# Kernel optimization log

Hardware: AMD Instinct MI355X
Metric: run time of the kernel (lower is better)

## Reference

```python
import jax, jax.numpy as jnp
import numpy as np

B, T, C = 2, 2048, 2048
H, Hk, D = 32, 4, 64
N_REP = H // Hk
THETA = 10000.0


def _rope_tables():
    inv_freq = 1.0 / (THETA ** (np.arange(0, D, 2, dtype=np.float64) / D))  # [D/2]
    t = np.arange(T, dtype=np.float64)
    freqs = np.outer(t, inv_freq)                # [T, D/2]
    emb = np.repeat(freqs, 2, axis=-1)           # interleaved [T, D]
    return jnp.asarray(np.cos(emb), jnp.float32), jnp.asarray(np.sin(emb), jnp.float32)


def setup_inputs() -> dict:
    key = jax.random.key(0)
    kx, kq, kk, kv, ko = jax.random.split(key, 5)
    scale = 0.02
    x = jax.random.normal(kx, (B, T, C), jnp.float32)
    wq = jax.random.normal(kq, (H * D, C), jnp.float32) * scale
    wk = jax.random.normal(kk, (Hk * D, C), jnp.float32) * scale
    wv = jax.random.normal(kv, (Hk * D, C), jnp.float32) * scale
    wo = jax.random.normal(ko, (C, H * D), jnp.float32) * scale
    cos, sin = _rope_tables()
    return {"x": x, "cos": cos, "sin": sin, "wq": wq, "wk": wk, "wv": wv, "wo": wo}


def _apply_rope(x, cos, sin):
    # x: [B, h, T, D]; cos/sin: [T, D] interleaved
    x1 = x[..., 0::2]
    x2 = x[..., 1::2]
    rot = jnp.stack([-x2, x1], axis=-1).reshape(x.shape)
    return x * cos[None, None] + rot * sin[None, None]


def reference(x, cos, sin, wq, wk, wv, wo):
    q = (x @ wq.T).reshape(B, T, H, D).transpose(0, 2, 1, 3)    # [B,H,T,D]
    k = (x @ wk.T).reshape(B, T, Hk, D).transpose(0, 2, 1, 3)   # [B,Hk,T,D]
    v = (x @ wv.T).reshape(B, T, Hk, D).transpose(0, 2, 1, 3)   # [B,Hk,T,D]
    q = _apply_rope(q, cos, sin)
    k = _apply_rope(k, cos, sin)
    # new_cache = (k, v) pre-repeat
    kr = jnp.repeat(k, N_REP, axis=1)                            # [B,H,T,D]
    vr = jnp.repeat(v, N_REP, axis=1)
    scores = jnp.einsum('bhtd,bhsd->bhts', q, kr) / jnp.sqrt(jnp.float32(D))
    mask = jnp.tril(jnp.ones((T, T), dtype=bool))                # causal (kv_cache is None)
    scores = jnp.where(mask, scores, jnp.finfo(scores.dtype).min)
    attn = jax.nn.softmax(scores, axis=-1)
    o = jnp.einsum('bhts,bhsd->bhtd', attn, vr)
    o = o.transpose(0, 2, 1, 3).reshape(B, T, H * D)
    return (o @ wo.T, k, v)
```

## Files before the change

kernel.cpp:

```cpp
#include <hip/hip_runtime.h>
#include <hip/hip_bf16.h>

#define B_ 2
#define T_ 2048
#define C_ 2048
#define H_ 32
#define HK_ 4
#define D_ 64

typedef __attribute__((ext_vector_type(4)))  float f32x4;
typedef __attribute__((ext_vector_type(2)))  float f32x2;
typedef __attribute__((ext_vector_type(16))) float f32x16;
typedef __attribute__((ext_vector_type(8)))  short bf16x8;

static __device__ __forceinline__ unsigned short f2bf(float f) {
  union { __hip_bfloat16 h; unsigned short s; } u;
  u.h = __float2bfloat16(f);
  return u.s;
}
static __device__ __forceinline__ float bf2f(unsigned short s) {
  union { unsigned int u; float f; } u; u.u = ((unsigned int)s) << 16; return u.f;
}
static __device__ __forceinline__ unsigned int cvtpk(float lo, float hi) {
  unsigned int r;
  asm("v_cvt_pk_bf16_f32 %0, %1, %2" : "=v"(r) : "v"(lo), "v"(hi));
  return r;
}

#define GLD16(gp, lp) __builtin_amdgcn_global_load_lds( \
    (const __attribute__((address_space(1))) unsigned int*)(gp), \
    (__attribute__((address_space(3))) unsigned int*)(unsigned int)(uintptr_t)(lp), 16, 0, 0)

__global__ void f32_to_bf16(const float* __restrict__ src, unsigned short* __restrict__ dst, int n4) {
  const int i = blockIdx.x * blockDim.x + threadIdx.x;
  if (i >= n4) return;
  f32x4 v = *(const f32x4*)(src + 4 * (size_t)i);
  ushort4 o;
  o.x = f2bf(v[0]); o.y = f2bf(v[1]); o.z = f2bf(v[2]); o.w = f2bf(v[3]);
  *(ushort4*)(dst + 4 * (size_t)i) = o;
}

template<bool BF16OUT>
__global__ __launch_bounds__(256, 3)
void gemm3(const unsigned short* __restrict__ A, const unsigned short* __restrict__ W,
           void* __restrict__ Cout, int M, int N, int K) {
  __shared__ unsigned short As[3][128 * 32];
  __shared__ unsigned short Ws[3][128 * 32];

  const int tid  = threadIdx.x;
  const int lane = tid & 63;
  const int w    = tid >> 6;
  const int wm   = w >> 1, wn = w & 1;
  const int g    = lane >> 4;
  const int lr   = lane & 15;

  const int bm = blockIdx.y * 128;
  const int bn = blockIdx.x * 128;

  const int srow = tid >> 2;
  const int sc   = (tid & 3) ^ (srow & 3);
  const unsigned short* Ag = A + (size_t)(bm + srow) * K + sc * 8;
  const unsigned short* Wg = W + (size_t)(bn + srow) * K + sc * 8;

#define STAGE3(buf, k0) do { \
    GLD16(Ag + (k0),                  &As[buf][       w * 512]); \
    GLD16(Ag + (size_t)64 * K + (k0), &As[buf][2048 + w * 512]); \
    GLD16(Wg + (k0),                  &Ws[buf][       w * 512]); \
    GLD16(Wg + (size_t)64 * K + (k0), &Ws[buf][2048 + w * 512]); \
  } while (0)

  f32x4 acc[4][4] = {};

  const int nt = K >> 5;
  STAGE3(0, 0);
  STAGE3(1, 32);

  for (int t = 0; t < nt; ++t) {
    if (t + 1 < nt) asm volatile("s_waitcnt vmcnt(4)" ::: "memory");
    else            asm volatile("s_waitcnt vmcnt(0)" ::: "memory");
    asm volatile("s_barrier" ::: "memory");

    if (t + 2 < nt) {
      const int nb = (t + 2) % 3;
      STAGE3(nb, (size_t)(t + 2) * 32);
    }

    const unsigned short* At = &As[t % 3][0];
    const unsigned short* Wt = &Ws[t % 3][0];

    bf16x8 af[4], wf[4];
#pragma unroll
    for (int m = 0; m < 4; m++) {
      const int row = wm * 64 + m * 16 + lr;
      af[m] = *(const bf16x8*)&At[row * 32 + ((g ^ (row & 3)) << 3)];
    }
#pragma unroll
    for (int n = 0; n < 4; n++) {
      const int row = wn * 64 + n * 16 + lr;
      wf[n] = *(const bf16x8*)&Wt[row * 32 + ((g ^ (row & 3)) << 3)];
    }
    __builtin_amdgcn_s_setprio(1);
#pragma unroll
    for (int m = 0; m < 4; m++)
#pragma unroll
      for (int n = 0; n < 4; n++)
        acc[m][n] = __builtin_amdgcn_mfma_f32_16x16x32_bf16(af[m], wf[n], acc[m][n], 0, 0, 0);
    __builtin_amdgcn_s_setprio(0);
  }
#undef STAGE3

#pragma unroll
  for (int m = 0; m < 4; m++) {
    const int row = bm + wm * 64 + m * 16 + g * 4;
#pragma unroll
    for (int n = 0; n < 4; n++) {
      const int col = bn + wn * 64 + n * 16 + lr;
#pragma unroll
      for (int r = 0; r < 4; r++) {
        if (BF16OUT)
          ((unsigned short*)Cout)[(size_t)(row + r) * N + col] = f2bf(acc[m][n][r]);
        else
          ((float*)Cout)[(size_t)(row + r) * N + col] = acc[m][n][r];
      }
    }
  }
}

__global__ void gqa_rope_q(const unsigned short* __restrict__ qkv,
                           const float* __restrict__ cosT,
                           const float* __restrict__ sinT,
                           unsigned short* __restrict__ qb) {
  const int idx = blockIdx.x * blockDim.x + threadIdx.x;
  const int i  = idx & 31;
  const int h  = (idx >> 5) & 31;
  const int bt = idx >> 10;
  const int t  = bt & (T_ - 1);
  const int b  = bt >> 11;

  const unsigned int qv = *(const unsigned int*)(qkv + (size_t)bt * 2560 + h * D_ + 2 * i);
  const float x1 = bf2f((unsigned short)(qv & 0xffff));
  const float x2 = bf2f((unsigned short)(qv >> 16));
  const float c = cosT[t * D_ + 2 * i];
  const float s = sinT[t * D_ + 2 * i];
  const float o0 = x1 * c - x2 * s;
  const float o1 = x2 * c + x1 * s;
  const size_t o = ((size_t)(b * H_ + h) * T_ + t) * D_ + 2 * i;
  *(unsigned int*)(qb + o) = (unsigned int)f2bf(o0) | ((unsigned int)f2bf(o1) << 16);
}

__global__ void gqa_rope_k(const unsigned short* __restrict__ qkv,
                           const float* __restrict__ cosT,
                           const float* __restrict__ sinT,
                           float* __restrict__ kout,
                           unsigned short* __restrict__ kb) {
  const int idx = blockIdx.x * blockDim.x + threadIdx.x;
  const int i  = idx & 31;
  const int hk = (idx >> 5) & 3;
  const int bt = idx >> 7;
  const int t  = bt & (T_ - 1);
  const int b  = bt >> 11;

  const unsigned int kv = *(const unsigned int*)(qkv + (size_t)bt * 2560 + 2048 + hk * D_ + 2 * i);
  const float x1 = bf2f((unsigned short)(kv & 0xffff));
  const float x2 = bf2f((unsigned short)(kv >> 16));
  const float c = cosT[t * D_ + 2 * i];
  const float s = sinT[t * D_ + 2 * i];
  const float o0 = x1 * c - x2 * s;
  const float o1 = x2 * c + x1 * s;
  const size_t o = ((size_t)(b * HK_ + hk) * T_ + t) * D_ + 2 * i;
  f32x2 ov; ov[0] = o0; ov[1] = o1;
  *(f32x2*)(kout + o) = ov;
  *(unsigned int*)(kb + o) = (unsigned int)f2bf(o0) | ((unsigned int)f2bf(o1) << 16);
}

__global__ void gqa_v_reorder(const unsigned short* __restrict__ qkv,
                              float* __restrict__ vout,
                              unsigned short* __restrict__ vt) {
  const int idx = blockIdx.x * blockDim.x + threadIdx.x;
  const int d  = idx & 63;
  const int hk = (idx >> 6) & 3;
  const int bt = idx >> 8;
  const int t  = bt & (T_ - 1);
  const int b  = bt >> 11;

  const unsigned short v = qkv[(size_t)bt * 2560 + 2304 + hk * D_ + d];
  vout[((size_t)(b * HK_ + hk) * T_ + t) * D_ + d] = bf2f(v);

  const int tm   = t & 15;
  const int tpos = (t & ~15) | ((tm & 3) + ((tm >> 3) << 2) + ((tm & 4) << 1));
  vt[((size_t)(b * HK_ + hk) * D_ + d) * T_ + tpos] = v;
}

__global__ __launch_bounds__(512, 4)
void gqa_attn4(const unsigned short* __restrict__ qb,
               const unsigned short* __restrict__ kb,
               const unsigned short* __restrict__ vt,
               unsigned short* __restrict__ ob) {
  __shared__ unsigned short Ks[3][4096];
  __shared__ unsigned short Vs[3][4096];

  const int tid  = threadIdx.x;
  const int lane = tid & 63;
  const int w    = tid >> 6;
  const int qi   = lane & 31;
  const int hi   = lane >> 5;

  const int qt = 63 - (int)(blockIdx.x >> 3);
  const int go = blockIdx.x & 7;
  const int b  = go >> 2;
  const int hk = go & 3;
  const int h  = hk * 8 + w;
  const int bh = b * H_ + h;

  const int qbase = qt * 32;
  const int qrow  = qbase + qi;

  const unsigned short* qptr = qb + ((size_t)bh * T_ + qrow) * D_ + 8 * hi;
  bf16x8 qf[4];
#pragma unroll
  for (int c = 0; c < 4; c++) qf[c] = *(const bf16x8*)(qptr + 16 * c);

  const int srow   = lane >> 3;
  const int schunk = (lane & 7) ^ srow;
  const int krow   = 8 * w + srow;
  const unsigned short* gK = kb + (size_t)(b * HK_ + hk) * T_ * D_ + (size_t)krow * D_ + schunk * 8;
  const unsigned short* gV = vt + (size_t)(b * HK_ + hk) * D_ * T_ + (size_t)krow * T_ + schunk * 8;
  unsigned short* ldsK = &Ks[0][w * 512];
  unsigned short* ldsV = &Vs[0][w * 512];

#define STAGE_KV(pp, kk0) do { \
    GLD16(gK + (size_t)(kk0) * D_, ldsK + (pp) * 4096); \
    GLD16(gV + (kk0),              ldsV + (pp) * 4096); \
  } while (0)

  f32x16 o0 = {}, o1 = {};
  float m = -1e30f, l = 0.f;
  float c1 = 0.f;
  const float SC   = 0.125f * 1.44269504089f;
  const float THRR = 44.3614195f;
  const int   swz  = qi & 7;

  const int nt = ((qbase + 31) >> 6) + 1;
  STAGE_KV(0, 0);
  if (nt > 1) STAGE_KV(1, 64);

  int p = 0;
  for (int it = 0; it < nt; ++it) {
    const int kb0 = it * 64;
    const bool last = (it == nt - 1);
    const bool has1 = (kb0 + 32 <= qbase + 31);

    asm volatile("s_waitcnt lgkmcnt(0)" ::: "memory");
    if (it + 1 < nt) asm volatile("s_waitcnt vmcnt(2)" ::: "memory");
    else             asm volatile("s_waitcnt vmcnt(0)" ::: "memory");
    asm volatile("s_barrier" ::: "memory");
    if (it + 2 < nt) STAGE_KV((p + 2 > 2) ? p - 1 : p + 2, kb0 + 128);

    const unsigned short* Kt = &Ks[0][0] + p * 4096;
    const unsigned short* Vt = &Vs[0][0] + p * 4096;

    f32x16 st0 = {}, st1 = {};
    __builtin_amdgcn_s_setprio(1);
#pragma unroll
    for (int c = 0; c < 4; c++) {
      bf16x8 kf = *(const bf16x8*)&Kt[qi * 64 + (((hi + 2 * c) ^ swz) << 3)];
      st0 = __builtin_amdgcn_mfma_f32_32x32x16_bf16(kf, qf[c], st0, 0, 0, 0);
    }
    if (!last || has1) {
#pragma unroll
      for (int c = 0; c < 4; c++) {
        bf16x8 kf = *(const bf16x8*)&Kt[(32 + qi) * 64 + (((hi + 2 * c) ^ swz) << 3)];
        st1 = __builtin_amdgcn_mfma_f32_32x32x16_bf16(kf, qf[c], st1, 0, 0, 0);
      }
    }
    __builtin_amdgcn_s_setprio(0);

    if (last) {
#pragma unroll
      for (int r = 0; r < 16; ++r) {
        const int key = kb0 + (r & 3) + 8 * (r >> 2) + 4 * hi;
        st0[r] = (key      <= qrow) ? st0[r] : -1e30f;
        st1[r] = (key + 32 <= qrow) ? st1[r] : -1e30f;
      }
    }

    float tmax = fmaxf(st0[0], st0[1]);
#pragma unroll
    for (int r = 2; r < 16; ++r) tmax = fmaxf(tmax, st0[r]);
#pragma unroll
    for (int r = 0; r < 16; ++r) tmax = fmaxf(tmax, st1[r]);
    tmax = fmaxf(tmax, __shfl_xor(tmax, 32));

    if (!__all(tmax <= m + THRR)) {
      const float mnew  = fmaxf(m, tmax);
      const float al    = __builtin_amdgcn_exp2f((m - mnew) * SC);
#pragma unroll
      for (int r = 0; r < 16; ++r) { o0[r] *= al; o1[r] *= al; }
      l *= al;
      m  = mnew;
      c1 = -m * SC;
    }

    float sum = 0.f;
#pragma unroll
    for (int r = 0; r < 16; ++r) { float pv = __builtin_amdgcn_exp2f(__builtin_fmaf(st0[r], SC, c1)); st0[r] = pv; sum += pv; }
#pragma unroll
    for (int r = 0; r < 16; ++r) { float pv = __builtin_amdgcn_exp2f(__builtin_fmaf(st1[r], SC, c1)); st1[r] = pv; sum += pv; }
    sum += __shfl_xor(sum, 32);
    l += sum;

    union U8 { bf16x8 v; unsigned int u[4]; };
    U8 pf[4];
#pragma unroll
    for (int j = 0; j < 4; ++j) {
      pf[0].u[j] = cvtpk(st0[2 * j],     st0[2 * j + 1]);
      pf[1].u[j] = cvtpk(st0[8 + 2 * j], st0[8 + 2 * j + 1]);
      pf[2].u[j] = cvtpk(st1[2 * j],     st1[2 * j + 1]);
      pf[3].u[j] = cvtpk(st1[8 + 2 * j], st1[8 + 2 * j + 1]);
    }

    const int ncf = (!last || has1) ? 4 : 2;
    __builtin_amdgcn_s_setprio(1);
#pragma unroll
    for (int dh = 0; dh < 2; ++dh) {
      const unsigned short* Vrow = &Vt[(dh * 32 + qi) * 64];
      f32x16 oc = dh ? o1 : o0;
#pragma unroll
      for (int c = 0; c < 4; ++c) {
        if (c >= ncf) break;
        bf16x8 vf = *(const bf16x8*)&Vrow[(((2 * c + hi) ^ swz) << 3)];
        oc = __builtin_amdgcn_mfma_f32_32x32x16_bf16(vf, pf[c].v, oc, 0, 0, 0);
      }
      if (dh) o1 = oc; else o0 = oc;
    }
    __builtin_amdgcn_s_setprio(0);

    p = (p > 1) ? 0 : p + 1;
  }

  const float inv = 1.0f / l;
  unsigned short* orow = ob + (size_t)(b * T_ + qrow) * (H_ * D_) + h * D_;
#pragma unroll
  for (int dh = 0; dh < 2; ++dh) {
    const f32x16 ov = dh ? o1 : o0;
#pragma unroll
    for (int rg = 0; rg < 4; ++rg) {
      const int d0 = 32 * dh + 8 * rg + 4 * hi;
      ushort4 pk;
      pk.x = f2bf(ov[4 * rg + 0] * inv);
      pk.y = f2bf(ov[4 * rg + 1] * inv);
      pk.z = f2bf(ov[4 * rg + 2] * inv);
      pk.w = f2bf(ov[4 * rg + 3] * inv);
      *(ushort4*)(orow + d0) = pk;
    }
  }
#undef STAGE_KV
}

extern "C" void kernel_launch(void* const* d_in, const int* in_sizes, int n_in,
                              void* d_out, int out_size, void* d_ws, size_t ws_size,
                              hipStream_t stream) {
  const float* x    = (const float*)d_in[0];
  const float* cosT = (const float*)d_in[1];
  const float* sinT = (const float*)d_in[2];
  const float* wq   = (const float*)d_in[3];
  const float* wk   = (const float*)d_in[4];
  const float* wv   = (const float*)d_in[5];
  const float* wo   = (const float*)d_in[6];

  float* y    = (float*)d_out;
  float* kout = (float*)d_out + (size_t)B_ * T_ * C_;
  float* vout = kout + (size_t)B_ * HK_ * T_ * D_;

  char* ws = (char*)d_ws;
  unsigned short* x_bf   = (unsigned short*)(ws);
  unsigned short* q_bf   = x_bf;
  unsigned short* wqkv   = (unsigned short*)(ws + 16777216);
  unsigned short* k_bf   = wqkv;
  unsigned short* v_t    = (unsigned short*)(ws + 18874368);
  unsigned short* qkv_bf = (unsigned short*)(ws + 27262976);
  unsigned short* o_bf   = qkv_bf;
  unsigned short* wo_bf  = (unsigned short*)(ws + 48234496);

  const int M = B_ * T_;

  f32_to_bf16<<<8192, 256, 0, stream>>>(x,  x_bf, 2097152);
  f32_to_bf16<<<4096, 256, 0, stream>>>(wq, wqkv,                 1048576);
  f32_to_bf16<<<512,  256, 0, stream>>>(wk, wqkv + 2048 * 2048,   131072);
  f32_to_bf16<<<512,  256, 0, stream>>>(wv, wqkv + 2304 * 2048,   131072);

  gemm3<true><<<dim3(2560 / 128, M / 128), 256, 0, stream>>>(x_bf, wqkv, qkv_bf, M, 2560, C_);

  gqa_rope_q<<<16384, 256, 0, stream>>>(qkv_bf, cosT, sinT, q_bf);
  gqa_rope_k<<<2048,  256, 0, stream>>>(qkv_bf, cosT, sinT, kout, k_bf);
  gqa_v_reorder<<<4096, 256, 0, stream>>>(qkv_bf, vout, v_t);

  f32_to_bf16<<<4096, 256, 0, stream>>>(wo, wo_bf, 1048576);

  gqa_attn4<<<512, 512, 0, stream>>>(q_bf, k_bf, v_t, o_bf);

  gemm3<false><<<dim3(C_ / 128, M / 128), 256, 0, stream>>>(o_bf, wo_bf, y, M, C_, H_ * D_);
}
```

Baseline: 209.2 us.

## Replace 128x128 triple-buffered GEMM with 128x256 double-buffered 512-thread GEMM

Both projection GEMMs now use a 128x256 block tile with 8 waves, a K-step of 64 instead of 32, and 8-way XOR swizzling in LDS. The pipeline drops from three buffers to two and waits for all loads (vmcnt(0)) before each barrier. The larger N tile raises reuse of the A tile and cuts the number of barriers per K. In exchange it uses more LDS per block and launches fewer blocks (320 and 256), which may leave parts of the 256-CU device underused and exposes load latency more.

```diff
diff --git a/kernel.cpp b/kernel.cpp
--- a/kernel.cpp
+++ b/kernel.cpp
@@ -41,73 +41,72 @@
 }
 
 template<bool BF16OUT>
-__global__ __launch_bounds__(256, 3)
-void gemm3(const unsigned short* __restrict__ A, const unsigned short* __restrict__ W,
-           void* __restrict__ Cout, int M, int N, int K) {
-  __shared__ unsigned short As[3][128 * 32];
-  __shared__ unsigned short Ws[3][128 * 32];
+__global__ __launch_bounds__(512, 2)
+void gemm256(const unsigned short* __restrict__ A, const unsigned short* __restrict__ W,
+             void* __restrict__ Cout, int M, int N, int K) {
+  __shared__ unsigned short As[2][128 * 64];
+  __shared__ unsigned short Bs[2][256 * 64];
 
   const int tid  = threadIdx.x;
   const int lane = tid & 63;
   const int w    = tid >> 6;
-  const int wm   = w >> 1, wn = w & 1;
+  const int wm   = w >> 2;
+  const int wn   = w & 3;
   const int g    = lane >> 4;
   const int lr   = lane & 15;
 
   const int bm = blockIdx.y * 128;
-  const int bn = blockIdx.x * 128;
-
-  const int srow = tid >> 2;
-  const int sc   = (tid & 3) ^ (srow & 3);
-  const unsigned short* Ag = A + (size_t)(bm + srow) * K + sc * 8;
-  const unsigned short* Wg = W + (size_t)(bn + srow) * K + sc * 8;
-
-#define STAGE3(buf, k0) do { \
-    GLD16(Ag + (k0),                  &As[buf][       w * 512]); \
-    GLD16(Ag + (size_t)64 * K + (k0), &As[buf][2048 + w * 512]); \
-    GLD16(Wg + (k0),                  &Ws[buf][       w * 512]); \
-    GLD16(Wg + (size_t)64 * K + (k0), &Ws[buf][2048 + w * 512]); \
+  const int bn = blockIdx.x * 256;
+
+  const int sr8 = lane >> 3;
+  const int sch = (lane & 7) ^ sr8;
+  const unsigned short* Ag = A + (size_t)(bm + w * 8 + sr8) * K + sch * 8;
+  const unsigned short* Wg = W + (size_t)(bn + w * 8 + sr8) * K + sch * 8;
+
+#define STG(buf, k0) do { \
+    GLD16(Ag + (k0),                   &As[buf][(      w * 8) * 64]); \
+    GLD16(Ag + (size_t)64  * K + (k0), &As[buf][(64  + w * 8) * 64]); \
+    GLD16(Wg + (k0),                   &Bs[buf][(      w * 8) * 64]); \
+    GLD16(Wg + (size_t)64  * K + (k0), &Bs[buf][(64  + w * 8) * 64]); \
+    GLD16(Wg + (size_t)128 * K + (k0), &Bs[buf][(128 + w * 8) * 64]); \
+    GLD16(Wg + (size_t)192 * K + (k0), &Bs[buf][(192 + w * 8) * 64]); \
   } while (0)
 
   f32x4 acc[4][4] = {};
-
-  const int nt = K >> 5;
-  STAGE3(0, 0);
-  STAGE3(1, 32);
+  const int nt = K >> 6;
+  STG(0, 0);
 
   for (int t = 0; t < nt; ++t) {
-    if (t + 1 < nt) asm volatile("s_waitcnt vmcnt(4)" ::: "memory");
-    else            asm volatile("s_waitcnt vmcnt(0)" ::: "memory");
-    asm volatile("s_barrier" ::: "memory");
-
-    if (t + 2 < nt) {
-      const int nb = (t + 2) % 3;
-      STAGE3(nb, (size_t)(t + 2) * 32);
-    }
-
-    const unsigned short* At = &As[t % 3][0];
-    const unsigned short* Wt = &Ws[t % 3][0];
-
-    bf16x8 af[4], wf[4];
-#pragma unroll
-    for (int m = 0; m < 4; m++) {
-      const int row = wm * 64 + m * 16 + lr;
-      af[m] = *(const bf16x8*)&At[row * 32 + ((g ^ (row & 3)) << 3)];
-    }
-#pragma unroll
-    for (int n = 0; n < 4; n++) {
-      const int row = wn * 64 + n * 16 + lr;
-      wf[n] = *(const bf16x8*)&Wt[row * 32 + ((g ^ (row & 3)) << 3)];
-    }
-    __builtin_amdgcn_s_setprio(1);
-#pragma unroll
-    for (int m = 0; m < 4; m++)
-#pragma unroll
-      for (int n = 0; n < 4; n++)
-        acc[m][n] = __builtin_amdgcn_mfma_f32_16x16x32_bf16(af[m], wf[n], acc[m][n], 0, 0, 0);
-    __builtin_amdgcn_s_setprio(0);
+    const int p = t & 1;
+    asm volatile("s_waitcnt vmcnt(0)" ::: "memory");
+    __builtin_amdgcn_s_barrier();
+    if (t + 1 < nt) STG(p ^ 1, (t + 1) << 6);
+
+    const unsigned short* At = &As[p][0];
+    const unsigned short* Bt = &Bs[p][0];
+#pragma unroll
+    for (int kh = 0; kh < 2; ++kh) {
+      bf16x8 af[4], wf[4];
+#pragma unroll
+      for (int m = 0; m < 4; m++) {
+        const int row = wm * 64 + m * 16 + lr;
+        af[m] = *(const bf16x8*)&At[row * 64 + (((g + 4 * kh) ^ (row & 7)) << 3)];
+      }
+#pragma unroll
+      for (int n = 0; n < 4; n++) {
+        const int row = wn * 64 + n * 16 + lr;
+        wf[n] = *(const bf16x8*)&Bt[row * 64 + (((g + 4 * kh) ^ (row & 7)) << 3)];
+      }
+      __builtin_amdgcn_s_setprio(1);
+#pragma unroll
+      for (int m = 0; m < 4; m++)
+#pragma unroll
+        for (int n = 0; n < 4; n++)
+          acc[m][n] = __builtin_amdgcn_mfma_f32_16x16x32_bf16(af[m], wf[n], acc[m][n], 0, 0, 0);
+      __builtin_amdgcn_s_setprio(0);
+    }
   }
-#undef STAGE3
+#undef STG
 
 #pragma unroll
   for (int m = 0; m < 4; m++) {
@@ -389,7 +388,7 @@
   f32_to_bf16<<<512,  256, 0, stream>>>(wk, wqkv + 2048 * 2048,   131072);
   f32_to_bf16<<<512,  256, 0, stream>>>(wv, wqkv + 2304 * 2048,   131072);
 
-  gemm3<true><<<dim3(2560 / 128, M / 128), 256, 0, stream>>>(x_bf, wqkv, qkv_bf, M, 2560, C_);
+  gemm256<true><<<dim3(2560 / 256, M / 128), 512, 0, stream>>>(x_bf, wqkv, qkv_bf, M, 2560, C_);
 
   gqa_rope_q<<<16384, 256, 0, stream>>>(qkv_bf, cosT, sinT, q_bf);
   gqa_rope_k<<<2048,  256, 0, stream>>>(qkv_bf, cosT, sinT, kout, k_bf);
@@ -399,5 +398,5 @@
 
   gqa_attn4<<<512, 512, 0, stream>>>(q_bf, k_bf, v_t, o_bf);
 
-  gemm3<false><<<dim3(C_ / 128, M / 128), 256, 0, stream>>>(o_bf, wo_bf, y, M, C_, H_ * D_);
-}
+  gemm256<false><<<dim3(C_ / 256, M / 128), 512, 0, stream>>>(o_bf, wo_bf, y, M, C_, H_ * D_);
+}
```

Result: no change. 206.8 us (-1.1%).

## Pair causal query tiles per attention block and merge weight conversion kernels

Applied to the files above, without the earlier changes.

The attention kernel now gives each block two query tiles, one from the far end and one from the near end of the causal range. Both tiles run over the same staged K/V tiles, so causal work is even across blocks and each K/V load is used twice. The grid shrinks to 256 blocks with launch bounds lowered to 2, which costs per-wave register pressure and occupancy. Separately, the five fp32-to-bf16 conversion launches become one combined kernel to cut launch overhead.

```diff
diff --git a/kernel.cpp b/kernel.cpp
--- a/kernel.cpp
+++ b/kernel.cpp
@@ -31,13 +31,25 @@
     (const __attribute__((address_space(1))) unsigned int*)(gp), \
     (__attribute__((address_space(3))) unsigned int*)(unsigned int)(uintptr_t)(lp), 16, 0, 0)
 
-__global__ void f32_to_bf16(const float* __restrict__ src, unsigned short* __restrict__ dst, int n4) {
+__global__ void conv_all(const float* __restrict__ x,  const float* __restrict__ wq,
+                         const float* __restrict__ wk, const float* __restrict__ wv,
+                         const float* __restrict__ wo,
+                         unsigned short* __restrict__ x_bf,
+                         unsigned short* __restrict__ wqkv,
+                         unsigned short* __restrict__ wo_bf) {
   const int i = blockIdx.x * blockDim.x + threadIdx.x;
-  if (i >= n4) return;
-  f32x4 v = *(const f32x4*)(src + 4 * (size_t)i);
+  const float* src;
+  unsigned short* dst;
+  int off;
+  if (i < 2097152)      { src = x;  dst = x_bf;                  off = i; }
+  else if (i < 3145728) { src = wq; dst = wqkv;                  off = i - 2097152; }
+  else if (i < 3276800) { src = wk; dst = wqkv + 2048 * 2048;    off = i - 3145728; }
+  else if (i < 3407872) { src = wv; dst = wqkv + 2304 * 2048;    off = i - 3276800; }
+  else                  { src = wo; dst = wo_bf;                 off = i - 3407872; }
+  f32x4 v = *(const f32x4*)(src + 4 * (size_t)off);
   ushort4 o;
   o.x = f2bf(v[0]); o.y = f2bf(v[1]); o.z = f2bf(v[2]); o.w = f2bf(v[3]);
-  *(ushort4*)(dst + 4 * (size_t)i) = o;
+  *(ushort4*)(dst + 4 * (size_t)off) = o;
 }
 
 template<bool BF16OUT>
@@ -191,8 +203,96 @@
   vt[((size_t)(b * HK_ + hk) * D_ + d) * T_ + tpos] = v;
 }
 
-__global__ __launch_bounds__(512, 4)
-void gqa_attn4(const unsigned short* __restrict__ qb,
+static __device__ __forceinline__ void attn_qstep(
+    const unsigned short* __restrict__ Kt, const unsigned short* __restrict__ Vt,
+    const bf16x8 (&qf)[4], f32x16& o0, f32x16& o1,
+    float& m, float& l, float& c1,
+    const int qrow, const int kb0, const bool last,
+    const int qi, const int hi, const int swz) {
+  const float SC   = 0.125f * 1.44269504089f;
+  const float THRR = 44.3614195f;
+  const int  qtop  = (qrow & ~31) + 31;
+  const bool has1  = (kb0 + 32 <= qtop);
+
+  f32x16 st0 = {}, st1 = {};
+  __builtin_amdgcn_s_setprio(1);
+#pragma unroll
+  for (int c = 0; c < 4; c++) {
+    bf16x8 kf = *(const bf16x8*)&Kt[qi * 64 + (((hi + 2 * c) ^ swz) << 3)];
+    st0 = __builtin_amdgcn_mfma_f32_32x32x16_bf16(kf, qf[c], st0, 0, 0, 0);
+  }
+  if (!last || has1) {
+#pragma unroll
+    for (int c = 0; c < 4; c++) {
+      bf16x8 kf = *(const bf16x8*)&Kt[(32 + qi) * 64 + (((hi + 2 * c) ^ swz) << 3)];
+      st1 = __builtin_amdgcn_mfma_f32_32x32x16_bf16(kf, qf[c], st1, 0, 0, 0);
+    }
+  }
+  __builtin_amdgcn_s_setprio(0);
+
+  if (last) {
+#pragma unroll
+    for (int r = 0; r < 16; ++r) {
+      const int key = kb0 + (r & 3) + 8 * (r >> 2) + 4 * hi;
+      st0[r] = (key      <= qrow) ? st0[r] : -1e30f;
+      st1[r] = (key + 32 <= qrow) ? st1[r] : -1e30f;
+    }
+  }
+
+  float tmax = fmaxf(st0[0], st0[1]);
+#pragma unroll
+  for (int r = 2; r < 16; ++r) tmax = fmaxf(tmax, st0[r]);
+#pragma unroll
+  for (int r = 0; r < 16; ++r) tmax = fmaxf(tmax, st1[r]);
+  tmax = fmaxf(tmax, __shfl_xor(tmax, 32));
+
+  if (!__all(tmax <= m + THRR)) {
+    const float mnew = fmaxf(m, tmax);
+    const float al   = __builtin_amdgcn_exp2f((m - mnew) * SC);
+#pragma unroll
+    for (int r = 0; r < 16; ++r) { o0[r] *= al; o1[r] *= al; }
+    l *= al;
+    m  = mnew;
+    c1 = -m * SC;
+  }
+
+  float sum = 0.f;
+#pragma unroll
+  for (int r = 0; r < 16; ++r) { float pv = __builtin_amdgcn_exp2f(__builtin_fmaf(st0[r], SC, c1)); st0[r] = pv; sum += pv; }
+#pragma unroll
+  for (int r = 0; r < 16; ++r) { float pv = __builtin_amdgcn_exp2f(__builtin_fmaf(st1[r], SC, c1)); st1[r] = pv; sum += pv; }
+  sum += __shfl_xor(sum, 32);
+  l += sum;
+
+  union U8 { bf16x8 v; unsigned int u[4]; };
+  U8 pf[4];
+#pragma unroll
+  for (int j = 0; j < 4; ++j) {
+    pf[0].u[j] = cvtpk(st0[2 * j],     st0[2 * j + 1]);
+    pf[1].u[j] = cvtpk(st0[8 + 2 * j], st0[8 + 2 * j + 1]);
+    pf[2].u[j] = cvtpk(st1[2 * j],     st1[2 * j + 1]);
+    pf[3].u[j] = cvtpk(st1[8 + 2 * j], st1[8 + 2 * j + 1]);
+  }
+
+  const int ncf = (!last || has1) ? 4 : 2;
+  __builtin_amdgcn_s_setprio(1);
+#pragma unroll
+  for (int dh = 0; dh < 2; ++dh) {
+    const unsigned short* Vrow = &Vt[(dh * 32 + qi) * 64];
+    f32x16 oc = dh ? o1 : o0;
+#pragma unroll
+    for (int c = 0; c < 4; ++c) {
+      if (c >= ncf) break;
+      bf16x8 vf = *(const bf16x8*)&Vrow[(((2 * c + hi) ^ swz) << 3)];
+      oc = __builtin_amdgcn_mfma_f32_32x32x16_bf16(vf, pf[c].v, oc, 0, 0, 0);
+    }
+    if (dh) o1 = oc; else o0 = oc;
+  }
+  __builtin_amdgcn_s_setprio(0);
+}
+
+__global__ __launch_bounds__(512, 2)
+void gqa_attn5(const unsigned short* __restrict__ qb,
                const unsigned short* __restrict__ kb,
                const unsigned short* __restrict__ vt,
                unsigned short* __restrict__ ob) {
@@ -205,20 +305,28 @@
   const int qi   = lane & 31;
   const int hi   = lane >> 5;
 
-  const int qt = 63 - (int)(blockIdx.x >> 3);
   const int go = blockIdx.x & 7;
+  const int pp = blockIdx.x >> 3;
   const int b  = go >> 2;
   const int hk = go & 3;
   const int h  = hk * 8 + w;
   const int bh = b * H_ + h;
 
-  const int qbase = qt * 32;
-  const int qrow  = qbase + qi;
-
-  const unsigned short* qptr = qb + ((size_t)bh * T_ + qrow) * D_ + 8 * hi;
-  bf16x8 qf[4];
-#pragma unroll
-  for (int c = 0; c < 4; c++) qf[c] = *(const bf16x8*)(qptr + 16 * c);
+  const int qbaseA = (63 - pp) * 32;
+  const int qbaseB = pp * 32;
+  const int qrowA  = qbaseA + qi;
+  const int qrowB  = qbaseB + qi;
+
+  bf16x8 qfA[4], qfB[4];
+  {
+    const unsigned short* qpA = qb + ((size_t)bh * T_ + qrowA) * D_ + 8 * hi;
+    const unsigned short* qpB = qb + ((size_t)bh * T_ + qrowB) * D_ + 8 * hi;
+#pragma unroll
+    for (int c = 0; c < 4; c++) {
+      qfA[c] = *(const bf16x8*)(qpA + 16 * c);
+      qfB[c] = *(const bf16x8*)(qpB + 16 * c);
+    }
+  }
 
   const int srow   = lane >> 3;
   const int schunk = (lane & 7) ^ srow;
@@ -228,130 +336,64 @@
   unsigned short* ldsK = &Ks[0][w * 512];
   unsigned short* ldsV = &Vs[0][w * 512];
 
-#define STAGE_KV(pp, kk0) do { \
-    GLD16(gK + (size_t)(kk0) * D_, ldsK + (pp) * 4096); \
-    GLD16(gV + (kk0),              ldsV + (pp) * 4096); \
+#define STAGE_KV(pbuf, kk0) do { \
+    GLD16(gK + (size_t)(kk0) * D_, ldsK + (pbuf) * 4096); \
+    GLD16(gV + (kk0),              ldsV + (pbuf) * 4096); \
   } while (0)
 
-  f32x16 o0 = {}, o1 = {};
-  float m = -1e30f, l = 0.f;
-  float c1 = 0.f;
-  const float SC   = 0.125f * 1.44269504089f;
-  const float THRR = 44.3614195f;
-  const int   swz  = qi & 7;
-
-  const int nt = ((qbase + 31) >> 6) + 1;
+  f32x16 o0A = {}, o1A = {}, o0B = {}, o1B = {};
+  float mA = -1e30f, lA = 0.f, c1A = 0.f;
+  float mB = -1e30f, lB = 0.f, c1B = 0.f;
+  const int swz = qi & 7;
+
+  const int ntA = ((qbaseA + 31) >> 6) + 1;
+  const int ntB = ((qbaseB + 31) >> 6) + 1;
+
   STAGE_KV(0, 0);
-  if (nt > 1) STAGE_KV(1, 64);
+  if (ntA > 1) STAGE_KV(1, 64);
 
   int p = 0;
-  for (int it = 0; it < nt; ++it) {
+  for (int it = 0; it < ntA; ++it) {
     const int kb0 = it * 64;
-    const bool last = (it == nt - 1);
-    const bool has1 = (kb0 + 32 <= qbase + 31);
 
     asm volatile("s_waitcnt lgkmcnt(0)" ::: "memory");
-    if (it + 1 < nt) asm volatile("s_waitcnt vmcnt(2)" ::: "memory");
-    else             asm volatile("s_waitcnt vmcnt(0)" ::: "memory");
+    if (it + 1 < ntA) asm volatile("s_waitcnt vmcnt(2)" ::: "memory");
+    else              asm volatile("s_waitcnt vmcnt(0)" ::: "memory");
     asm volatile("s_barrier" ::: "memory");
-    if (it + 2 < nt) STAGE_KV((p + 2 > 2) ? p - 1 : p + 2, kb0 + 128);
+    if (it + 2 < ntA) STAGE_KV((p + 2 > 2) ? p - 1 : p + 2, kb0 + 128);
 
     const unsigned short* Kt = &Ks[0][0] + p * 4096;
     const unsigned short* Vt = &Vs[0][0] + p * 4096;
 
-    f32x16 st0 = {}, st1 = {};
-    __builtin_amdgcn_s_setprio(1);
-#pragma unroll
-    for (int c = 0; c < 4; c++) {
-      bf16x8 kf = *(const bf16x8*)&Kt[qi * 64 + (((hi + 2 * c) ^ swz) << 3)];
-      st0 = __builtin_amdgcn_mfma_f32_32x32x16_bf16(kf, qf[c], st0, 0, 0, 0);
-    }
-    if (!last || has1) {
-#pragma unroll
-      for (int c = 0; c < 4; c++) {
-        bf16x8 kf = *(const bf16x8*)&Kt[(32 + qi) * 64 + (((hi + 2 * c) ^ swz) << 3)];
-        st1 = __builtin_amdgcn_mfma_f32_32x32x16_bf16(kf, qf[c], st1, 0, 0, 0);
-      }
-    }
-    __builtin_amdgcn_s_setprio(0);
-
-    if (last) {
-#pragma unroll
-      for (int r = 0; r < 16; ++r) {
-        const int key = kb0 + (r & 3) + 8 * (r >> 2) + 4 * hi;
-        st0[r] = (key      <= qrow) ? st0[r] : -1e30f;
-        st1[r] = (key + 32 <= qrow) ? st1[r] : -1e30f;
-      }
-    }
-
-    float tmax = fmaxf(st0[0], st0[1]);
-#pragma unroll
-    for (int r = 2; r < 16; ++r) tmax = fmaxf(tmax, st0[r]);
-#pragma unroll
-    for (int r = 0; r < 16; ++r) tmax = fmaxf(tmax, st1[r]);
-    tmax = fmaxf(tmax, __shfl_xor(tmax, 32));
-
-    if (!__all(tmax <= m + THRR)) {
-      const float mnew  = fmaxf(m, tmax);
-      const float al    = __builtin_amdgcn_exp2f((m - mnew) * SC);
-#pragma unroll
-      for (int r = 0; r < 16; ++r) { o0[r] *= al; o1[r] *= al; }
-      l *= al;
-      m  = mnew;
-      c1 = -m * SC;
-    }
-
-    float sum = 0.f;
-#pragma unroll
-    for (int r = 0; r < 16; ++r) { float pv = __builtin_amdgcn_exp2f(__builtin_fmaf(st0[r], SC, c1)); st0[r] = pv; sum += pv; }
-#pragma unroll
-    for (int r = 0; r < 16; ++r) { float pv = __builtin_amdgcn_exp2f(__builtin_fmaf(st1[r], SC, c1)); st1[r] = pv; sum += pv; }
-    sum += __shfl_xor(sum, 32);
-    l += sum;
-
-    union U8 { bf16x8 v; unsigned int u[4]; };
-    U8 pf[4];
-#pragma unroll
-    for (int j = 0; j < 4; ++j) {
-      pf[0].u[j] = cvtpk(st0[2 * j],     st0[2 * j + 1]);
-      pf[1].u[j] = cvtpk(st0[8 + 2 * j], st0[8 + 2 * j + 1]);
-      pf[2].u[j] = cvtpk(st1[2 * j],     st1[2 * j + 1]);
-      pf[3].u[j] = cvtpk(st1[8 + 2 * j], st1[8 + 2 * j + 1]);
-    }
-
-    const int ncf = (!last || has1) ? 4 : 2;
-    __builtin_amdgcn_s_setprio(1);
-#pragma unroll
-    for (int dh = 0; dh < 2; ++dh) {
-      const unsigned short* Vrow = &Vt[(dh * 32 + qi) * 64];
-      f32x16 oc = dh ? o1 : o0;
-#pragma unroll
-      for (int c = 0; c < 4; ++c) {
-        if (c >= ncf) break;
-        bf16x8 vf = *(const bf16x8*)&Vrow[(((2 * c + hi) ^ swz) << 3)];
-        oc = __builtin_amdgcn_mfma_f32_32x32x16_bf16(vf, pf[c].v, oc, 0, 0, 0);
-      }
-      if (dh) o1 = oc; else o0 = oc;
-    }
-    __builtin_amdgcn_s_setprio(0);
+    attn_qstep(Kt, Vt, qfA, o0A, o1A, mA, lA, c1A, qrowA, kb0, it == ntA - 1, qi, hi, swz);
+    if (it < ntB)
+      attn_qstep(Kt, Vt, qfB, o0B, o1B, mB, lB, c1B, qrowB, kb0, it == ntB - 1, qi, hi, swz);
 
     p = (p > 1) ? 0 : p + 1;
   }
 
-  const float inv = 1.0f / l;
-  unsigned short* orow = ob + (size_t)(b * T_ + qrow) * (H_ * D_) + h * D_;
+  const float invA = 1.0f / lA;
+  const float invB = 1.0f / lB;
+  unsigned short* orowA = ob + (size_t)(b * T_ + qrowA) * (H_ * D_) + h * D_;
+  unsigned short* orowB = ob + (size_t)(b * T_ + qrowB) * (H_ * D_) + h * D_;
 #pragma unroll
   for (int dh = 0; dh < 2; ++dh) {
-    const f32x16 ov = dh ? o1 : o0;
+    const f32x16 ovA = dh ? o1A : o0A;
+    const f32x16 ovB = dh ? o1B : o0B;
 #pragma unroll
     for (int rg = 0; rg < 4; ++rg) {
       const int d0 = 32 * dh + 8 * rg + 4 * hi;
-      ushort4 pk;
-      pk.x = f2bf(ov[4 * rg + 0] * inv);
-      pk.y = f2bf(ov[4 * rg + 1] * inv);
-      pk.z = f2bf(ov[4 * rg + 2] * inv);
-      pk.w = f2bf(ov[4 * rg + 3] * inv);
-      *(ushort4*)(orow + d0) = pk;
+      ushort4 pkA, pkB;
+      pkA.x = f2bf(ovA[4 * rg + 0] * invA);
+      pkA.y = f2bf(ovA[4 * rg + 1] * invA);
+      pkA.z = f2bf(ovA[4 * rg + 2] * invA);
+      pkA.w = f2bf(ovA[4 * rg + 3] * invA);
+      pkB.x = f2bf(ovB[4 * rg + 0] * invB);
+      pkB.y = f2bf(ovB[4 * rg + 1] * invB);
+      pkB.z = f2bf(ovB[4 * rg + 2] * invB);
+      pkB.w = f2bf(ovB[4 * rg + 3] * invB);
+      *(ushort4*)(orowA + d0) = pkA;
+      *(ushort4*)(orowB + d0) = pkB;
     }
   }
 #undef STAGE_KV
@@ -384,10 +426,7 @@
 
   const int M = B_ * T_;
 
-  f32_to_bf16<<<8192, 256, 0, stream>>>(x,  x_bf, 2097152);
-  f32_to_bf16<<<4096, 256, 0, stream>>>(wq, wqkv,                 1048576);
-  f32_to_bf16<<<512,  256, 0, stream>>>(wk, wqkv + 2048 * 2048,   131072);
-  f32_to_bf16<<<512,  256, 0, stream>>>(wv, wqkv + 2304 * 2048,   131072);
+  conv_all<<<17408, 256, 0, stream>>>(x, wq, wk, wv, wo, x_bf, wqkv, wo_bf);
 
   gemm3<true><<<dim3(2560 / 128, M / 128), 256, 0, stream>>>(x_bf, wqkv, qkv_bf, M, 2560, C_);
 
@@ -395,9 +434,7 @@
   gqa_rope_k<<<2048,  256, 0, stream>>>(qkv_bf, cosT, sinT, kout, k_bf);
   gqa_v_reorder<<<4096, 256, 0, stream>>>(qkv_bf, vout, v_t);
 
-  f32_to_bf16<<<4096, 256, 0, stream>>>(wo, wo_bf, 1048576);
-
-  gqa_attn4<<<512, 512, 0, stream>>>(q_bf, k_bf, v_t, o_bf);
+  gqa_attn5<<<256, 512, 0, stream>>>(q_bf, k_bf, v_t, o_bf);
 
   gemm3<false><<<dim3(C_ / 128, M / 128), 256, 0, stream>>>(o_bf, wo_bf, y, M, C_, H_ * D_);
 }
```

Measured after the change: 198.8 us. -4.9%, faster.
